# Kernel tuning notes

Hardware: AMD Instinct MI355X
Metric: run time of the kernel (lower is better)

## Reference

```python
import jax, jax.numpy as jnp
import numpy as np

B, N, K, C, CE, H = 2, 2048, 48, 128, 128, 128
IN = 2 * C + CE  # 384
AGG_SCALE = 30.0
LN_EPS = 1e-5


def setup_inputs() -> dict:
    key = jax.random.key(0)
    ks = jax.random.split(key, 12)
    inp = {
        "node_h": jax.random.normal(ks[0], (B, N, C), jnp.float32),
        "edge_h": jax.random.normal(ks[1], (B, N, K, CE), jnp.float32),
        "edge_index": jax.random.randint(ks[2], (B, N, K), 0, N, jnp.int64),
        # message MLP: Linear(IN,H) GELU Linear(H,H) GELU Linear(H,C)
        "W1": jax.random.normal(ks[3], (IN, H), jnp.float32) / np.sqrt(IN),
        "b1": jnp.zeros((H,), jnp.float32),
        "W2": jax.random.normal(ks[4], (H, H), jnp.float32) / np.sqrt(H),
        "b2": jnp.zeros((H,), jnp.float32),
        "W3": jax.random.normal(ks[5], (H, C), jnp.float32) / np.sqrt(H),
        "b3": jnp.zeros((C,), jnp.float32),
        "Wu": jax.random.normal(ks[6], (C, C), jnp.float32) / np.sqrt(C),
        "bu": jnp.zeros((C,), jnp.float32),
        "ln_g": jnp.ones((C,), jnp.float32),
        "ln_b": jnp.zeros((C,), jnp.float32),
    }
    return inp


def _layer_norm(x, g, b):
    mu = jnp.mean(x, axis=-1, keepdims=True)
    var = jnp.var(x, axis=-1, keepdims=True)
    return (x - mu) * jax.lax.rsqrt(var + LN_EPS) * g + b


def _gelu(x):
    return jax.nn.gelu(x, approximate=False)  # torch nn.GELU default (erf)


def reference(node_h, edge_h, edge_index, W1, b1, W2, b2, W3, b3, Wu, bu, ln_g, ln_b):
    b, n, k = edge_index.shape
    c = node_h.shape[-1]
    # gather neighbor node features: (B,N,K,C)
    node_j = jnp.take_along_axis(
        node_h, edge_index.reshape(b, n * k)[..., None], axis=1
    ).reshape(b, n, k, c)
    node_i = jnp.broadcast_to(node_h[:, :, None, :], (b, n, k, c))
    edge_packed = jnp.concatenate([node_i, node_j, edge_h], axis=-1)  # (B,N,K,IN)
    # message MLP
    h = _gelu(edge_packed @ W1 + b1)
    h = _gelu(h @ W2 + b2)
    messages = (h @ W3 + b3).sum(axis=-2) / AGG_SCALE  # (B,N,C)
    # dropout is identity in eval mode
    updated_nodes = _layer_norm(node_h + messages, ln_g, ln_b)
    node_updates = updated_nodes @ Wu + bu
    out = _layer_norm(node_h + node_updates, ln_g, ln_b)
    return out
```

## Files before the change

kernel.cpp:

```cpp
#include <hip/hip_runtime.h>
#include <hip/hip_bf16.h>
#include <math.h>

#define Bn   2
#define Nn   2048
#define Kn   48
#define Cn   128
#define G2   16

typedef short bf16x8 __attribute__((ext_vector_type(8)));
typedef float f32x4  __attribute__((ext_vector_type(4)));

#if __has_builtin(__builtin_amdgcn_cvt_pk_bf16_f32)
#define HAS_PK 1
#endif

__device__ __forceinline__ short f2bf(float f) {
  union { float f; unsigned u; } v; v.f = f;
  unsigned r = v.u + 0x7fffu + ((v.u >> 16) & 1u);
  return (short)(r >> 16);
}

__device__ __forceinline__ unsigned pk2(float a, float b) {
#ifdef HAS_PK
  auto p = __builtin_amdgcn_cvt_pk_bf16_f32(a, b);
  return __builtin_bit_cast(unsigned, p);
#else
  return (unsigned)(unsigned short)f2bf(a) | ((unsigned)(unsigned short)f2bf(b) << 16);
#endif
}

__device__ __forceinline__ float gelu_f(float x) {
  float z = x * (-2.3021991f - 0.10294200f * x * x);
  float e = __builtin_amdgcn_exp2f(z);
  return x * __builtin_amdgcn_rcpf(1.0f + e);
}

__global__ void pack_weights(const float* __restrict__ W1,
                             const float* __restrict__ W2,
                             const float* __restrict__ W3,
                             const float* __restrict__ Wu,
                             short* __restrict__ ws) {
  int tid = blockIdx.x * blockDim.x + threadIdx.x;
  if (tid >= 192 * 64) return;
  int lane = tid & 63;
  int tile = tid >> 6;
  const float* W; short* dst;
  if (tile < 32)       { W = W1;         dst = ws; }
  else if (tile < 96)  { W = W1 + 16384; dst = ws + 16384; tile -= 32; }
  else if (tile < 128) { W = W2;         dst = ws + 49152; tile -= 96; }
  else if (tile < 160) { W = W3;         dst = ws + 65536; tile -= 128; }
  else                 { W = Wu;         dst = ws + 81920; tile -= 160; }
  int kt = tile >> 3, nt = tile & 7;
  int n  = nt * 16 + (lane & 15);
  int k0 = kt * 32 + (lane >> 4) * 8;
  union { short s[8]; bf16x8 v; } u8;
#pragma unroll
  for (int j = 0; j < 8; j++) u8.s[j] = f2bf(W[(k0 + j) * 128 + n]);
  *reinterpret_cast<bf16x8*>(dst + (tile << 9) + lane * 8) = u8.v;
}

__global__ __launch_bounds__(512, 6)
void node_update_kernel(const float* __restrict__ node_h,
                        const float* __restrict__ edge_h,
                        const int*   __restrict__ edge_index,
                        const short* __restrict__ wpack,
                        const float* __restrict__ b1,
                        const float* __restrict__ b2,
                        float* __restrict__ hs_out) {
  __shared__ __align__(16) char smem[25472];
  short* Xs    = (short*)smem;
  short* H1s   = (short*)smem;
  short* nhb   = (short*)(smem + 24576);
  int*   idx_s = (int*)  (smem + 25088);

  const int tid  = threadIdx.x;
  const int n0   = blockIdx.x * 2;
  const int bb   = n0 >> 11;
  const int lane = tid & 63;
  const int wave = tid >> 6;
  const int lr   = lane & 15;
  const int lq   = lane >> 4;

  const short* W1i = wpack;
  const short* W1e = wpack + 16384;
  const short* W2p = wpack + 49152;

  bf16x8 w1i[4];
#pragma unroll
  for (int kt = 0; kt < 4; kt++)
    w1i[kt] = *reinterpret_cast<const bf16x8*>(W1i + ((kt * 8 + wave) << 9) + lane * 8);
  const int colw = wave * 16 + lr;
  const float b1v = b1[colw];
  const float b2v = b2[colw];

  if (tid < 256) {
    nhb[tid] = f2bf(node_h[(size_t)n0 * Cn + tid]);
  } else if (tid < 352) {
    idx_s[tid - 256] = edge_index[n0 * Kn + (tid - 256)];
  }
  __syncthreads();

  const int gw = tid & 15;
  const int gr = tid >> 4;

  float4 na[3], nb[3];
#pragma unroll
  for (int k = 0; k < 3; k++) {
    int r = gr + k * 32;
    const float* src = node_h + (size_t)(bb * Nn + idx_s[r]) * Cn + gw * 8;
    na[k] = *reinterpret_cast<const float4*>(src);
    nb[k] = *reinterpret_cast<const float4*>(src + 4);
  }

  f32x4 accY[2] = {};
#pragma unroll
  for (int kt = 0; kt < 4; kt++) {
    bf16x8 avA = {}, avB = {};
    if (lr == 0) {
      avA = *reinterpret_cast<const bf16x8*>(&nhb[kt * 32 + lq * 8]);
      avB = *reinterpret_cast<const bf16x8*>(&nhb[128 + kt * 32 + lq * 8]);
    }
    accY[0] = __builtin_amdgcn_mfma_f32_16x16x32_bf16(avA, w1i[kt], accY[0], 0, 0, 0);
    accY[1] = __builtin_amdgcn_mfma_f32_16x16x32_bf16(avB, w1i[kt], accY[1], 0, 0, 0);
  }
  const float yiA = __shfl(accY[0][0], lr) + b1v;
  const float yiB = __shfl(accY[1][0], lr) + b1v;

#pragma unroll
  for (int k = 0; k < 3; k++) {
    int r = gr + k * 32;
    uint4 p;
    p.x = pk2(na[k].x, na[k].y); p.y = pk2(na[k].z, na[k].w);
    p.z = pk2(nb[k].x, nb[k].y); p.w = pk2(nb[k].z, nb[k].w);
    *reinterpret_cast<uint4*>(&Xs[r * 128 + ((gw ^ (r & 7)) << 3)]) = p;
  }
  __syncthreads();

  bf16x8 w1a[4];
#pragma unroll
  for (int kt = 0; kt < 4; kt++)
    w1a[kt] = *reinterpret_cast<const bf16x8*>(W1e + ((kt * 8 + wave) << 9) + lane * 8);
  float4 ea[3], eb[3];
#pragma unroll
  for (int k = 0; k < 3; k++) {
    int r = gr + k * 32;
    const float* src = edge_h + ((size_t)n0 * Kn + r) * Cn + gw * 8;
    ea[k] = *reinterpret_cast<const float4*>(src);
    eb[k] = *reinterpret_cast<const float4*>(src + 4);
  }

  f32x4 acc[6] = {};
#pragma unroll
  for (int kt = 0; kt < 4; kt++) {
    int sw = (((kt * 4 + lq) ^ (lr & 7)) << 3);
#pragma unroll
    for (int m = 0; m < 6; m++) {
      bf16x8 a = *reinterpret_cast<const bf16x8*>(&Xs[(m * 16 + lr) * 128 + sw]);
      acc[m] = __builtin_amdgcn_mfma_f32_16x16x32_bf16(a, w1a[kt], acc[m], 0, 0, 0);
    }
  }
  __syncthreads();

#pragma unroll
  for (int k = 0; k < 3; k++) {
    int r = gr + k * 32;
    uint4 p;
    p.x = pk2(ea[k].x, ea[k].y); p.y = pk2(ea[k].z, ea[k].w);
    p.z = pk2(eb[k].x, eb[k].y); p.w = pk2(eb[k].z, eb[k].w);
    *reinterpret_cast<uint4*>(&Xs[r * 128 + ((gw ^ (r & 7)) << 3)]) = p;
  }
  __syncthreads();

#pragma unroll
  for (int kt = 0; kt < 4; kt++) {
    bf16x8 bf = *reinterpret_cast<const bf16x8*>(W1e + (((kt + 4) * 8 + wave) << 9) + lane * 8);
    int sw = (((kt * 4 + lq) ^ (lr & 7)) << 3);
#pragma unroll
    for (int m = 0; m < 6; m++) {
      bf16x8 a = *reinterpret_cast<const bf16x8*>(&Xs[(m * 16 + lr) * 128 + sw]);
      acc[m] = __builtin_amdgcn_mfma_f32_16x16x32_bf16(a, bf, acc[m], 0, 0, 0);
    }
  }
  __syncthreads();

  {
    int g = colw >> 3, cl = colw & 7;
#pragma unroll
    for (int mt = 0; mt < 6; mt++) {
      float yi = (mt < 3) ? yiA : yiB;
      int r0 = mt * 16 + lq * 4;
      float g0 = gelu_f(acc[mt][0] + yi);
      float g1 = gelu_f(acc[mt][1] + yi);
      float g2 = gelu_f(acc[mt][2] + yi);
      float g3 = gelu_f(acc[mt][3] + yi);
      unsigned p01 = pk2(g0, g1), p23 = pk2(g2, g3);
      H1s[(r0 + 0) * 128 + ((g ^ ((r0 + 0) & 7)) << 3) + cl] = (short)(p01 & 0xffff);
      H1s[(r0 + 1) * 128 + ((g ^ ((r0 + 1) & 7)) << 3) + cl] = (short)(p01 >> 16);
      H1s[(r0 + 2) * 128 + ((g ^ ((r0 + 2) & 7)) << 3) + cl] = (short)(p23 & 0xffff);
      H1s[(r0 + 3) * 128 + ((g ^ ((r0 + 3) & 7)) << 3) + cl] = (short)(p23 >> 16);
    }
  }
  __syncthreads();

  f32x4 acc2[6] = {};
#pragma unroll
  for (int kt = 0; kt < 4; kt++) {
    bf16x8 bf = *reinterpret_cast<const bf16x8*>(W2p + ((kt * 8 + wave) << 9) + lane * 8);
    int sw = (((kt * 4 + lq) ^ (lr & 7)) << 3);
#pragma unroll
    for (int m = 0; m < 6; m++) {
      bf16x8 a = *reinterpret_cast<const bf16x8*>(&H1s[(m * 16 + lr) * 128 + sw]);
      acc2[m] = __builtin_amdgcn_mfma_f32_16x16x32_bf16(a, bf, acc2[m], 0, 0, 0);
    }
  }
  {
    float sA = 0.f, sB = 0.f;
#pragma unroll
    for (int mt = 0; mt < 3; mt++)
#pragma unroll
      for (int r = 0; r < 4; r++) {
        sA += gelu_f(acc2[mt][r] + b2v);
        sB += gelu_f(acc2[mt + 3][r] + b2v);
      }
    sA += __shfl_xor(sA, 16);
    sA += __shfl_xor(sA, 32);
    sB += __shfl_xor(sB, 16);
    sB += __shfl_xor(sB, 32);
    if (lq == 0) {
      hs_out[(size_t)n0 * Cn + colw]       = sA;
      hs_out[(size_t)(n0 + 1) * Cn + colw] = sB;
    }
  }
}

__global__ __launch_bounds__(256, 4)
void tail_kernel(const float* __restrict__ node_h,
                 const short* __restrict__ wpack,
                 const float* __restrict__ b3,
                 const float* __restrict__ bu,
                 const float* __restrict__ ln_g,
                 const float* __restrict__ ln_b,
                 float* __restrict__ out) {
  __shared__ __align__(16) char sm2[24832];
  short* hsB = (short*)sm2;
  float* nhr = (float*)(sm2 + 4096);
  float* xs  = (float*)(sm2 + 12288);
  short* usB = (short*)(sm2 + 20736);

  const int tid  = threadIdx.x;
  const int lane = tid & 63;
  const int wave = tid >> 6;
  const int lr   = lane & 15;
  const int lq   = lane >> 4;
  const int n0   = blockIdx.x * G2;

  const short* W3p = wpack + 65536;
  const short* Wup = wpack + 81920;

  {
    int row = tid >> 4, seg = tid & 15;
    const float* p = node_h + (size_t)(n0 + row) * Cn + seg * 8;
    float4 a0 = *reinterpret_cast<const float4*>(p);
    float4 a1 = *reinterpret_cast<const float4*>(p + 4);
    *reinterpret_cast<float4*>(&nhr[row * 128 + seg * 8])     = a0;
    *reinterpret_cast<float4*>(&nhr[row * 128 + seg * 8 + 4]) = a1;
    const float* q = out + (size_t)(n0 + row) * Cn + seg * 8;
    float4 c0 = *reinterpret_cast<const float4*>(q);
    float4 c1 = *reinterpret_cast<const float4*>(q + 4);
    uint4 pk;
    pk.x = pk2(c0.x, c0.y); pk.y = pk2(c0.z, c0.w);
    pk.z = pk2(c1.x, c1.y); pk.w = pk2(c1.z, c1.w);
    *reinterpret_cast<uint4*>(&hsB[row * 128 + ((seg ^ (row & 7)) << 3)]) = pk;
  }
  __syncthreads();

  f32x4 am[2] = {};
#pragma unroll
  for (int kt = 0; kt < 4; kt++) {
    bf16x8 av = *reinterpret_cast<const bf16x8*>(&hsB[lr * 128 + (((kt * 4 + lq) ^ (lr & 7)) << 3)]);
    bf16x8 bv0 = *reinterpret_cast<const bf16x8*>(W3p + ((kt * 8 + wave * 2 + 0) << 9) + lane * 8);
    bf16x8 bv1 = *reinterpret_cast<const bf16x8*>(W3p + ((kt * 8 + wave * 2 + 1) << 9) + lane * 8);
    am[0] = __builtin_amdgcn_mfma_f32_16x16x32_bf16(av, bv0, am[0], 0, 0, 0);
    am[1] = __builtin_amdgcn_mfma_f32_16x16x32_bf16(av, bv1, am[1], 0, 0, 0);
  }
#pragma unroll
  for (int j = 0; j < 2; j++) {
    int col = (wave * 2 + j) * 16 + lr;
    float bb = 48.0f * b3[col];
#pragma unroll
    for (int r = 0; r < 4; r++) {
      int row = lq * 4 + r;
      xs[row * 132 + col] = nhr[row * 128 + col] + (am[j][r] + bb) * (1.0f / 30.0f);
    }
  }
  __syncthreads();

  const float lg1 = ln_g[lane],      lb1v = ln_b[lane];
  const float lg2 = ln_g[lane + 64], lb2v = ln_b[lane + 64];
#pragma unroll
  for (int s = 0; s < 4; s++) {
    int row = wave * 4 + s;
    float v1 = xs[row * 132 + lane];
    float v2 = xs[row * 132 + lane + 64];
    float s1 = v1 + v2, s2 = v1 * v1 + v2 * v2;
#pragma unroll
    for (int off = 32; off >= 1; off >>= 1) {
      s1 += __shfl_xor(s1, off);
      s2 += __shfl_xor(s2, off);
    }
    float mu = s1 * (1.f / 128.f);
    float var = s2 * (1.f / 128.f) - mu * mu;
    float rstd = rsqrtf(var + 1e-5f);
    unsigned u12 = pk2((v1 - mu) * rstd * lg1 + lb1v,
                       (v2 - mu) * rstd * lg2 + lb2v);
    int sw = (row & 7);
    usB[row * 128 + (((lane >> 3) ^ sw) << 3) + (lane & 7)]       = (short)(u12 & 0xffff);
    usB[row * 128 + ((((lane >> 3) + 8) ^ sw) << 3) + (lane & 7)] = (short)(u12 >> 16);
  }
  __syncthreads();

  f32x4 au[2] = {};
#pragma unroll
  for (int kt = 0; kt < 4; kt++) {
    bf16x8 av = *reinterpret_cast<const bf16x8*>(&usB[lr * 128 + (((kt * 4 + lq) ^ (lr & 7)) << 3)]);
    bf16x8 bv0 = *reinterpret_cast<const bf16x8*>(Wup + ((kt * 8 + wave * 2 + 0) << 9) + lane * 8);
    bf16x8 bv1 = *reinterpret_cast<const bf16x8*>(Wup + ((kt * 8 + wave * 2 + 1) << 9) + lane * 8);
    au[0] = __builtin_amdgcn_mfma_f32_16x16x32_bf16(av, bv0, au[0], 0, 0, 0);
    au[1] = __builtin_amdgcn_mfma_f32_16x16x32_bf16(av, bv1, au[1], 0, 0, 0);
  }
  __syncthreads();
#pragma unroll
  for (int j = 0; j < 2; j++) {
    int col = (wave * 2 + j) * 16 + lr;
    float bb = bu[col];
#pragma unroll
    for (int r = 0; r < 4; r++) {
      int row = lq * 4 + r;
      xs[row * 132 + col] = nhr[row * 128 + col] + au[j][r] + bb;
    }
  }
  __syncthreads();

#pragma unroll
  for (int s = 0; s < 4; s++) {
    int row = wave * 4 + s;
    float v1 = xs[row * 132 + lane];
    float v2 = xs[row * 132 + lane + 64];
    float s1 = v1 + v2, s2 = v1 * v1 + v2 * v2;
#pragma unroll
    for (int off = 32; off >= 1; off >>= 1) {
      s1 += __shfl_xor(s1, off);
      s2 += __shfl_xor(s2, off);
    }
    float mu = s1 * (1.f / 128.f);
    float var = s2 * (1.f / 128.f) - mu * mu;
    float rstd = rsqrtf(var + 1e-5f);
    out[(size_t)(n0 + row) * Cn + lane]      = (v1 - mu) * rstd * lg1 + lb1v;
    out[(size_t)(n0 + row) * Cn + lane + 64] = (v2 - mu) * rstd * lg2 + lb2v;
  }
}

extern "C" void kernel_launch(void* const* d_in, const int* in_sizes, int n_in,
                              void* d_out, int out_size, void* d_ws, size_t ws_size,
                              hipStream_t stream) {
  const float* node_h     = (const float*)d_in[0];
  const float* edge_h     = (const float*)d_in[1];
  const int*   edge_index = (const int*)  d_in[2];
  const float* W1 = (const float*)d_in[3];
  const float* b1 = (const float*)d_in[4];
  const float* W2 = (const float*)d_in[5];
  const float* b2 = (const float*)d_in[6];
  const float* W3 = (const float*)d_in[7];
  const float* b3 = (const float*)d_in[8];
  const float* Wu = (const float*)d_in[9];
  const float* bu = (const float*)d_in[10];
  const float* ln_g = (const float*)d_in[11];
  const float* ln_b = (const float*)d_in[12];
  float* out   = (float*)d_out;
  short* wpack = (short*)d_ws;

  pack_weights<<<48, 256, 0, stream>>>(W1, W2, W3, Wu, wpack);
  node_update_kernel<<<(Bn * Nn) / 2, 512, 0, stream>>>(
      node_h, edge_h, edge_index, wpack, b1, b2, out);
  tail_kernel<<<(Bn * Nn) / G2, 256, 0, stream>>>(
      node_h, wpack, b3, bu, ln_g, ln_b, out);
}
```

Baseline: 202.7 us.

## Process four node pairs per block with register-prefetched software pipeline

Each block of the node update kernel now loops over four node pairs instead of handling one. It prefetches the next pair's edge features, neighbor gathers, indices and node rows into registers and double-buffered LDS while the current pair's MFMAs run. Edge features get their own LDS buffer, which doubles shared memory and lowers the occupancy hint from 6 to 4 blocks per CU. The aim is to hide global load latency behind compute and spread fixed per-block setup cost. The risks are lower occupancy, more register pressure and fewer blocks (512) to spread across the CUs.

Measured after the change: 250.3 us. +23.5%, slower.

```diff
diff --git a/kernel.cpp b/kernel.cpp
--- a/kernel.cpp
+++ b/kernel.cpp
@@ -7,6 +7,7 @@
 #define Kn   48
 #define Cn   128
 #define G2   16
+#define NP   4
 
 typedef short bf16x8 __attribute__((ext_vector_type(8)));
 typedef float f32x4  __attribute__((ext_vector_type(4)));
@@ -60,7 +61,7 @@
   *reinterpret_cast<bf16x8*>(dst + (tile << 9) + lane * 8) = u8.v;
 }
 
-__global__ __launch_bounds__(512, 6)
+__global__ __launch_bounds__(512, 4)
 void node_update_kernel(const float* __restrict__ node_h,
                         const float* __restrict__ edge_h,
                         const int*   __restrict__ edge_index,
@@ -68,19 +69,21 @@
                         const float* __restrict__ b1,
                         const float* __restrict__ b2,
                         float* __restrict__ hs_out) {
-  __shared__ __align__(16) char smem[25472];
-  short* Xs    = (short*)smem;
-  short* H1s   = (short*)smem;
-  short* nhb   = (short*)(smem + 24576);
-  int*   idx_s = (int*)  (smem + 25088);
+  __shared__ __align__(16) char smem[50944];
+  short* Xs   = (short*)smem;
+  short* H1s  = (short*)smem;
+  short* Es   = (short*)(smem + 24576);
+  short* nhb2 = (short*)(smem + 49152);
+  int*   idx2 = (int*)  (smem + 50176);
 
   const int tid  = threadIdx.x;
-  const int n0   = blockIdx.x * 2;
-  const int bb   = n0 >> 11;
+  const int pair0 = blockIdx.x * NP;
   const int lane = tid & 63;
   const int wave = tid >> 6;
   const int lr   = lane & 15;
   const int lq   = lane >> 4;
+  const int gw   = tid & 15;
+  const int gr   = tid >> 4;
 
   const short* W1i = wpack;
   const short* W1e = wpack + 16384;
@@ -94,143 +97,171 @@
   const float b1v = b1[colw];
   const float b2v = b2[colw];
 
+  float4 ea[3], eb[3];
+  {
+    const int n0 = pair0 * 2;
+#pragma unroll
+    for (int k = 0; k < 3; k++) {
+      int r = gr + k * 32;
+      const float* src = edge_h + ((size_t)n0 * Kn + r) * Cn + gw * 8;
+      ea[k] = *reinterpret_cast<const float4*>(src);
+      eb[k] = *reinterpret_cast<const float4*>(src + 4);
+    }
+  }
   if (tid < 256) {
-    nhb[tid] = f2bf(node_h[(size_t)n0 * Cn + tid]);
+    nhb2[tid] = f2bf(node_h[(size_t)(pair0 * 2) * Cn + tid]);
   } else if (tid < 352) {
-    idx_s[tid - 256] = edge_index[n0 * Kn + (tid - 256)];
-  }
-  __syncthreads();
-
-  const int gw = tid & 15;
-  const int gr = tid >> 4;
-
+    idx2[tid - 256] = edge_index[(pair0 * 2) * Kn + (tid - 256)];
+  }
+  __syncthreads();
   float4 na[3], nb[3];
-#pragma unroll
-  for (int k = 0; k < 3; k++) {
-    int r = gr + k * 32;
-    const float* src = node_h + (size_t)(bb * Nn + idx_s[r]) * Cn + gw * 8;
-    na[k] = *reinterpret_cast<const float4*>(src);
-    nb[k] = *reinterpret_cast<const float4*>(src + 4);
-  }
-
-  f32x4 accY[2] = {};
-#pragma unroll
-  for (int kt = 0; kt < 4; kt++) {
-    bf16x8 avA = {}, avB = {};
-    if (lr == 0) {
-      avA = *reinterpret_cast<const bf16x8*>(&nhb[kt * 32 + lq * 8]);
-      avB = *reinterpret_cast<const bf16x8*>(&nhb[128 + kt * 32 + lq * 8]);
-    }
-    accY[0] = __builtin_amdgcn_mfma_f32_16x16x32_bf16(avA, w1i[kt], accY[0], 0, 0, 0);
-    accY[1] = __builtin_amdgcn_mfma_f32_16x16x32_bf16(avB, w1i[kt], accY[1], 0, 0, 0);
-  }
-  const float yiA = __shfl(accY[0][0], lr) + b1v;
-  const float yiB = __shfl(accY[1][0], lr) + b1v;
-
-#pragma unroll
-  for (int k = 0; k < 3; k++) {
-    int r = gr + k * 32;
-    uint4 p;
-    p.x = pk2(na[k].x, na[k].y); p.y = pk2(na[k].z, na[k].w);
-    p.z = pk2(nb[k].x, nb[k].y); p.w = pk2(nb[k].z, nb[k].w);
-    *reinterpret_cast<uint4*>(&Xs[r * 128 + ((gw ^ (r & 7)) << 3)]) = p;
-  }
-  __syncthreads();
-
-  bf16x8 w1a[4];
-#pragma unroll
-  for (int kt = 0; kt < 4; kt++)
-    w1a[kt] = *reinterpret_cast<const bf16x8*>(W1e + ((kt * 8 + wave) << 9) + lane * 8);
-  float4 ea[3], eb[3];
-#pragma unroll
-  for (int k = 0; k < 3; k++) {
-    int r = gr + k * 32;
-    const float* src = edge_h + ((size_t)n0 * Kn + r) * Cn + gw * 8;
-    ea[k] = *reinterpret_cast<const float4*>(src);
-    eb[k] = *reinterpret_cast<const float4*>(src + 4);
-  }
-
-  f32x4 acc[6] = {};
-#pragma unroll
-  for (int kt = 0; kt < 4; kt++) {
-    int sw = (((kt * 4 + lq) ^ (lr & 7)) << 3);
-#pragma unroll
-    for (int m = 0; m < 6; m++) {
-      bf16x8 a = *reinterpret_cast<const bf16x8*>(&Xs[(m * 16 + lr) * 128 + sw]);
-      acc[m] = __builtin_amdgcn_mfma_f32_16x16x32_bf16(a, w1a[kt], acc[m], 0, 0, 0);
-    }
-  }
-  __syncthreads();
-
-#pragma unroll
-  for (int k = 0; k < 3; k++) {
-    int r = gr + k * 32;
-    uint4 p;
-    p.x = pk2(ea[k].x, ea[k].y); p.y = pk2(ea[k].z, ea[k].w);
-    p.z = pk2(eb[k].x, eb[k].y); p.w = pk2(eb[k].z, eb[k].w);
-    *reinterpret_cast<uint4*>(&Xs[r * 128 + ((gw ^ (r & 7)) << 3)]) = p;
-  }
-  __syncthreads();
-
-#pragma unroll
-  for (int kt = 0; kt < 4; kt++) {
-    bf16x8 bf = *reinterpret_cast<const bf16x8*>(W1e + (((kt + 4) * 8 + wave) << 9) + lane * 8);
-    int sw = (((kt * 4 + lq) ^ (lr & 7)) << 3);
-#pragma unroll
-    for (int m = 0; m < 6; m++) {
-      bf16x8 a = *reinterpret_cast<const bf16x8*>(&Xs[(m * 16 + lr) * 128 + sw]);
-      acc[m] = __builtin_amdgcn_mfma_f32_16x16x32_bf16(a, bf, acc[m], 0, 0, 0);
-    }
-  }
-  __syncthreads();
-
   {
-    int g = colw >> 3, cl = colw & 7;
-#pragma unroll
-    for (int mt = 0; mt < 6; mt++) {
-      float yi = (mt < 3) ? yiA : yiB;
-      int r0 = mt * 16 + lq * 4;
-      float g0 = gelu_f(acc[mt][0] + yi);
-      float g1 = gelu_f(acc[mt][1] + yi);
-      float g2 = gelu_f(acc[mt][2] + yi);
-      float g3 = gelu_f(acc[mt][3] + yi);
-      unsigned p01 = pk2(g0, g1), p23 = pk2(g2, g3);
-      H1s[(r0 + 0) * 128 + ((g ^ ((r0 + 0) & 7)) << 3) + cl] = (short)(p01 & 0xffff);
-      H1s[(r0 + 1) * 128 + ((g ^ ((r0 + 1) & 7)) << 3) + cl] = (short)(p01 >> 16);
-      H1s[(r0 + 2) * 128 + ((g ^ ((r0 + 2) & 7)) << 3) + cl] = (short)(p23 & 0xffff);
-      H1s[(r0 + 3) * 128 + ((g ^ ((r0 + 3) & 7)) << 3) + cl] = (short)(p23 >> 16);
-    }
-  }
-  __syncthreads();
-
-  f32x4 acc2[6] = {};
-#pragma unroll
-  for (int kt = 0; kt < 4; kt++) {
-    bf16x8 bf = *reinterpret_cast<const bf16x8*>(W2p + ((kt * 8 + wave) << 9) + lane * 8);
-    int sw = (((kt * 4 + lq) ^ (lr & 7)) << 3);
-#pragma unroll
-    for (int m = 0; m < 6; m++) {
-      bf16x8 a = *reinterpret_cast<const bf16x8*>(&H1s[(m * 16 + lr) * 128 + sw]);
-      acc2[m] = __builtin_amdgcn_mfma_f32_16x16x32_bf16(a, bf, acc2[m], 0, 0, 0);
-    }
-  }
-  {
-    float sA = 0.f, sB = 0.f;
-#pragma unroll
-    for (int mt = 0; mt < 3; mt++)
-#pragma unroll
-      for (int r = 0; r < 4; r++) {
-        sA += gelu_f(acc2[mt][r] + b2v);
-        sB += gelu_f(acc2[mt + 3][r] + b2v);
-      }
-    sA += __shfl_xor(sA, 16);
-    sA += __shfl_xor(sA, 32);
-    sB += __shfl_xor(sB, 16);
-    sB += __shfl_xor(sB, 32);
-    if (lq == 0) {
-      hs_out[(size_t)n0 * Cn + colw]       = sA;
-      hs_out[(size_t)(n0 + 1) * Cn + colw] = sB;
-    }
+    const int n0 = pair0 * 2;
+    const int bb = n0 >> 11;
+#pragma unroll
+    for (int k = 0; k < 3; k++) {
+      int r = gr + k * 32;
+      const float* src = node_h + ((size_t)(bb * Nn) + idx2[r]) * Cn + gw * 8;
+      na[k] = *reinterpret_cast<const float4*>(src);
+      nb[k] = *reinterpret_cast<const float4*>(src + 4);
+    }
+  }
+
+#pragma unroll
+  for (int i = 0; i < NP; i++) {
+    const int n0  = (pair0 + i) * 2;
+    const int cur = i & 1;
+    const int nxt = cur ^ 1;
+
+    if (i + 1 < NP) {
+      if (tid < 256) {
+        nhb2[nxt * 256 + tid] = f2bf(node_h[(size_t)(n0 + 2) * Cn + tid]);
+      } else if (tid < 352) {
+        idx2[nxt * 96 + (tid - 256)] = edge_index[(n0 + 2) * Kn + (tid - 256)];
+      }
+    }
+    f32x4 accY[2] = {};
+#pragma unroll
+    for (int kt = 0; kt < 4; kt++) {
+      bf16x8 avA = {}, avB = {};
+      if (lr == 0) {
+        avA = *reinterpret_cast<const bf16x8*>(&nhb2[cur * 256 + kt * 32 + lq * 8]);
+        avB = *reinterpret_cast<const bf16x8*>(&nhb2[cur * 256 + 128 + kt * 32 + lq * 8]);
+      }
+      accY[0] = __builtin_amdgcn_mfma_f32_16x16x32_bf16(avA, w1i[kt], accY[0], 0, 0, 0);
+      accY[1] = __builtin_amdgcn_mfma_f32_16x16x32_bf16(avB, w1i[kt], accY[1], 0, 0, 0);
+    }
+    const float yiA = __shfl(accY[0][0], lr) + b1v;
+    const float yiB = __shfl(accY[1][0], lr) + b1v;
+#pragma unroll
+    for (int k = 0; k < 3; k++) {
+      int r = gr + k * 32;
+      uint4 p;
+      p.x = pk2(na[k].x, na[k].y); p.y = pk2(na[k].z, na[k].w);
+      p.z = pk2(nb[k].x, nb[k].y); p.w = pk2(nb[k].z, nb[k].w);
+      *reinterpret_cast<uint4*>(&Xs[r * 128 + ((gw ^ (r & 7)) << 3)]) = p;
+    }
+    __syncthreads();
+
+    f32x4 acc[6] = {};
+#pragma unroll
+    for (int kt = 0; kt < 4; kt++) {
+      bf16x8 bf = *reinterpret_cast<const bf16x8*>(W1e + ((kt * 8 + wave) << 9) + lane * 8);
+      int sw = (((kt * 4 + lq) ^ (lr & 7)) << 3);
+#pragma unroll
+      for (int m = 0; m < 6; m++) {
+        bf16x8 a = *reinterpret_cast<const bf16x8*>(&Xs[(m * 16 + lr) * 128 + sw]);
+        acc[m] = __builtin_amdgcn_mfma_f32_16x16x32_bf16(a, bf, acc[m], 0, 0, 0);
+      }
+    }
+#pragma unroll
+    for (int k = 0; k < 3; k++) {
+      int r = gr + k * 32;
+      uint4 p;
+      p.x = pk2(ea[k].x, ea[k].y); p.y = pk2(ea[k].z, ea[k].w);
+      p.z = pk2(eb[k].x, eb[k].y); p.w = pk2(eb[k].z, eb[k].w);
+      *reinterpret_cast<uint4*>(&Es[r * 128 + ((gw ^ (r & 7)) << 3)]) = p;
+    }
+    __syncthreads();
+
+    if (i + 1 < NP) {
+      const int n2 = n0 + 2;
+      const int bb2 = n2 >> 11;
+#pragma unroll
+      for (int k = 0; k < 3; k++) {
+        int r = gr + k * 32;
+        const float* esrc = edge_h + ((size_t)n2 * Kn + r) * Cn + gw * 8;
+        ea[k] = *reinterpret_cast<const float4*>(esrc);
+        eb[k] = *reinterpret_cast<const float4*>(esrc + 4);
+      }
+#pragma unroll
+      for (int k = 0; k < 3; k++) {
+        int r = gr + k * 32;
+        const float* nsrc = node_h + ((size_t)(bb2 * Nn) + idx2[nxt * 96 + r]) * Cn + gw * 8;
+        na[k] = *reinterpret_cast<const float4*>(nsrc);
+        nb[k] = *reinterpret_cast<const float4*>(nsrc + 4);
+      }
+      __builtin_amdgcn_sched_barrier(0);
+    }
+#pragma unroll
+    for (int kt = 0; kt < 4; kt++) {
+      bf16x8 bf = *reinterpret_cast<const bf16x8*>(W1e + (((kt + 4) * 8 + wave) << 9) + lane * 8);
+      int sw = (((kt * 4 + lq) ^ (lr & 7)) << 3);
+#pragma unroll
+      for (int m = 0; m < 6; m++) {
+        bf16x8 a = *reinterpret_cast<const bf16x8*>(&Es[(m * 16 + lr) * 128 + sw]);
+        acc[m] = __builtin_amdgcn_mfma_f32_16x16x32_bf16(a, bf, acc[m], 0, 0, 0);
+      }
+    }
+    {
+      int g = colw >> 3, cl = colw & 7;
+#pragma unroll
+      for (int mt = 0; mt < 6; mt++) {
+        float yi = (mt < 3) ? yiA : yiB;
+        int r0 = mt * 16 + lq * 4;
+        float g0 = gelu_f(acc[mt][0] + yi);
+        float g1 = gelu_f(acc[mt][1] + yi);
+        float g2 = gelu_f(acc[mt][2] + yi);
+        float g3 = gelu_f(acc[mt][3] + yi);
+        unsigned p01 = pk2(g0, g1), p23 = pk2(g2, g3);
+        H1s[(r0 + 0) * 128 + ((g ^ ((r0 + 0) & 7)) << 3) + cl] = (short)(p01 & 0xffff);
+        H1s[(r0 + 1) * 128 + ((g ^ ((r0 + 1) & 7)) << 3) + cl] = (short)(p01 >> 16);
+        H1s[(r0 + 2) * 128 + ((g ^ ((r0 + 2) & 7)) << 3) + cl] = (short)(p23 & 0xffff);
+        H1s[(r0 + 3) * 128 + ((g ^ ((r0 + 3) & 7)) << 3) + cl] = (short)(p23 >> 16);
+      }
+    }
+    __syncthreads();
+
+    f32x4 acc2[6] = {};
+#pragma unroll
+    for (int kt = 0; kt < 4; kt++) {
+      bf16x8 bf = *reinterpret_cast<const bf16x8*>(W2p + ((kt * 8 + wave) << 9) + lane * 8);
+      int sw = (((kt * 4 + lq) ^ (lr & 7)) << 3);
+#pragma unroll
+      for (int m = 0; m < 6; m++) {
+        bf16x8 a = *reinterpret_cast<const bf16x8*>(&H1s[(m * 16 + lr) * 128 + sw]);
+        acc2[m] = __builtin_amdgcn_mfma_f32_16x16x32_bf16(a, bf, acc2[m], 0, 0, 0);
+      }
+    }
+    {
+      float sA = 0.f, sB = 0.f;
+#pragma unroll
+      for (int mt = 0; mt < 3; mt++)
+#pragma unroll
+        for (int r = 0; r < 4; r++) {
+          sA += gelu_f(acc2[mt][r] + b2v);
+          sB += gelu_f(acc2[mt + 3][r] + b2v);
+        }
+      sA += __shfl_xor(sA, 16);
+      sA += __shfl_xor(sA, 32);
+      sB += __shfl_xor(sB, 16);
+      sB += __shfl_xor(sB, 32);
+      if (lq == 0) {
+        hs_out[(size_t)n0 * Cn + colw]       = sA;
+        hs_out[(size_t)(n0 + 1) * Cn + colw] = sB;
+      }
+    }
+    __syncthreads();
   }
 }
 
@@ -381,7 +412,7 @@
   short* wpack = (short*)d_ws;
 
   pack_weights<<<48, 256, 0, stream>>>(W1, W2, W3, Wu, wpack);
-  node_update_kernel<<<(Bn * Nn) / 2, 512, 0, stream>>>(
+  node_update_kernel<<<(Bn * Nn) / (2 * NP), 512, 0, stream>>>(
       node_h, edge_h, edge_index, wpack, b1, b2, out);
   tail_kernel<<<(Bn * Nn) / G2, 256, 0, stream>>>(
       node_h, wpack, b3, bu, ln_g, ln_b, out);
```
